# Performance work log

Measured on AMD Instinct MI355X. Metric: run time of the kernel, lower is better.

The kernel has to match this reference:

```python
import jax, jax.numpy as jnp
import numpy as np

B, S, D_MODEL = 8, 1024, 1024
N_HEADS, N_KV_HEADS, HEAD_DIM = 16, 8, 64
ROPE_THETA = 10000.0
LN_EPS = 1e-12


def setup_inputs() -> dict:
    key = jax.random.key(0)
    ks = jax.random.split(key, 6)
    sc = 0.02
    return {
        "hidden_states": jax.random.normal(ks[0], (B, S, D_MODEL), jnp.float32),
        "Wq": jax.random.normal(ks[1], (D_MODEL, N_HEADS * HEAD_DIM), jnp.float32) * sc,
        "bq": jnp.zeros((N_HEADS * HEAD_DIM,), jnp.float32),
        "Wk": jax.random.normal(ks[2], (D_MODEL, N_KV_HEADS * HEAD_DIM), jnp.float32) * sc,
        "bk": jnp.zeros((N_KV_HEADS * HEAD_DIM,), jnp.float32),
        "Wv": jax.random.normal(ks[3], (D_MODEL, N_KV_HEADS * HEAD_DIM), jnp.float32) * sc,
        "bv": jnp.zeros((N_KV_HEADS * HEAD_DIM,), jnp.float32),
        "Wo": jax.random.normal(ks[4], (N_HEADS * HEAD_DIM, D_MODEL), jnp.float32) * sc,
        "bo": jnp.zeros((D_MODEL,), jnp.float32),
        "ln_gamma": jnp.ones((D_MODEL,), jnp.float32),
        "ln_beta": jnp.zeros((D_MODEL,), jnp.float32),
    }


def _rope_tables(seq_len, dim, dtype):
    # lucidrains RotaryEmbedding: inv_freq over even indices, interleaved pairs
    inv_freq = 1.0 / (ROPE_THETA ** (jnp.arange(0, dim, 2, dtype=jnp.float32) / dim))
    angles = jnp.arange(seq_len, dtype=jnp.float32)[:, None] * inv_freq[None, :]  # [S, dim/2]
    return jnp.cos(angles).astype(dtype), jnp.sin(angles).astype(dtype)


def _apply_rope(x, cos, sin):
    # x: [B, S, H, D]; rotate interleaved pairs (x0,x1),(x2,x3),...
    x1 = x[..., 0::2]
    x2 = x[..., 1::2]
    c = cos[None, :, None, :]
    s = sin[None, :, None, :]
    y1 = x1 * c - x2 * s
    y2 = x1 * s + x2 * c
    return jnp.stack([y1, y2], axis=-1).reshape(x.shape)


def reference(hidden_states, Wq, bq, Wk, bk, Wv, bv, Wo, bo, ln_gamma, ln_beta):
    b, s, _ = hidden_states.shape
    q = (hidden_states @ Wq + bq).reshape(b, s, N_HEADS, HEAD_DIM)
    k = (hidden_states @ Wk + bk).reshape(b, s, N_KV_HEADS, HEAD_DIM)
    v = (hidden_states @ Wv + bv).reshape(b, s, N_KV_HEADS, HEAD_DIM)

    cos, sin = _rope_tables(s, HEAD_DIM, hidden_states.dtype)
    q = _apply_rope(q, cos, sin)
    k = _apply_rope(k, cos, sin)

    # GQA: repeat_interleave kv heads to match query heads (factor 2)
    rep = N_HEADS // N_KV_HEADS
    k = jnp.repeat(k, rep, axis=2)  # [B, S, H, D]
    v = jnp.repeat(v, rep, axis=2)

    scale = 1.0 / jnp.sqrt(jnp.asarray(HEAD_DIM, hidden_states.dtype))
    scores = jnp.einsum('bqhd,bkhd->bhqk', q * scale, k)  # [B, H, S, S]
    probs = jax.nn.softmax(scores, axis=-1)
    attn = jnp.einsum('bhqk,bkhd->bqhd', probs, v).reshape(b, s, N_HEADS * HEAD_DIM)

    out = attn @ Wo + bo
    resid = out + hidden_states
    mu = jnp.mean(resid, axis=-1, keepdims=True)
    var = jnp.mean(jnp.square(resid - mu), axis=-1, keepdims=True)
    normed = (resid - mu) * jax.lax.rsqrt(var + LN_EPS)
    return normed * ln_gamma + ln_beta
```

## Files before the change

kernel.cpp:

```cpp
#include <hip/hip_runtime.h>
#include <math.h>
#include <stdint.h>

typedef unsigned short u16;
typedef __bf16 bf16x8 __attribute__((ext_vector_type(8)));
typedef float f32x4 __attribute__((ext_vector_type(4)));

typedef const __attribute__((address_space(1))) void gv_t;
typedef __attribute__((address_space(3))) void lv_t;

__device__ __forceinline__ u16 f2bf(float f) {
    unsigned u = __builtin_bit_cast(unsigned, f);
    return (u16)((u + 0x7FFFu + ((u >> 16) & 1u)) >> 16);
}
__device__ __forceinline__ float bf2f(u16 h) {
    return __builtin_bit_cast(float, (unsigned)h << 16);
}
__device__ __forceinline__ void gll16(const void* g, void* l) {
    __builtin_amdgcn_global_load_lds((gv_t*)(uintptr_t)g,
                                     (lv_t*)(unsigned)(uintptr_t)l, 16, 0, 0);
}

__global__ __launch_bounds__(256) void cvt_bf16_kernel(
    const float* __restrict__ in, u16* __restrict__ out, int n4)
{
    int i = blockIdx.x * 256 + threadIdx.x;
    if (i >= n4) return;
    float4 f = ((const float4*)in)[i];
    ushort4 o = make_ushort4(f2bf(f.x), f2bf(f.y), f2bf(f.z), f2bf(f.w));
    ((ushort4*)out)[i] = o;
}

__global__ __launch_bounds__(256) void cvt_t4_kernel(
    const float* __restrict__ w0, const float* __restrict__ w1,
    const float* __restrict__ w2, const float* __restrict__ w3,
    u16* __restrict__ o0, u16* __restrict__ o1,
    u16* __restrict__ o2, u16* __restrict__ o3)
{
    __shared__ u16 t[64][65];
    const float* in; u16* out; int N;
    switch (blockIdx.z) {
        case 0: in = w0; out = o0; N = 1024; break;
        case 1: in = w1; out = o1; N = 512;  break;
        case 2: in = w2; out = o2; N = 512;  break;
        default: in = w3; out = o3; N = 1024; break;
    }
    int kb = blockIdx.y * 64, nb = blockIdx.x * 64;
    if (nb >= N) return;
    int tid = threadIdx.x;
#pragma unroll
    for (int c = 0; c < 16; ++c) {
        int id = c * 256 + tid;
        int r = id >> 6, n = id & 63;
        t[n][r] = f2bf(in[(size_t)(kb + r) * N + nb + n]);
    }
    __syncthreads();
#pragma unroll
    for (int c = 0; c < 16; ++c) {
        int id = c * 256 + tid;
        int r = id >> 6, n = id & 63;
        out[(size_t)(nb + r) * 1024 + kb + n] = t[r][n];
    }
}

template<int MODE>
__global__ __launch_bounds__(256) void gemm_mfma(
    const u16* __restrict__ A, const u16* __restrict__ Bt,
    const float* __restrict__ b0, const float* __restrict__ b1,
    const float* __restrict__ b2,
    const float* __restrict__ resid, float* __restrict__ Cf,
    u16* __restrict__ Qo, u16* __restrict__ Ko, u16* __restrict__ Vto,
    int N, int K)
{
    __shared__ __align__(16) u16 Asl[128 * 64];
    __shared__ __align__(16) u16 Bsl[128 * 64];
    const int tid = threadIdx.x, lane = tid & 63, w = tid >> 6;
    const int quad = lane >> 4, l16 = lane & 15;
    const int bm = blockIdx.y * 128, bn = blockIdx.x * 128;
    const int wm = (w >> 1) * 64, wn = (w & 1) * 64;

    f32x4 acc[4][4] = {};

    const int dr = lane >> 3;
    const int dcs = (((lane & 7) ^ dr) << 3);
    const u16* Ag = &A[(size_t)(bm + w * 32 + dr) * K + dcs];
    const u16* Bg = &Bt[(size_t)(bn + w * 32 + dr) * K + dcs];
    u16* Al = &Asl[(w * 32) * 64];
    u16* Bl = &Bsl[(w * 32) * 64];

    const int sw = l16 & 7;

    for (int k0 = 0; k0 < K; k0 += 64) {
#pragma unroll
        for (int c = 0; c < 4; ++c) {
            gll16(Ag + (size_t)(c * 8) * K + k0, Al + c * 8 * 64);
            gll16(Bg + (size_t)(c * 8) * K + k0, Bl + c * 8 * 64);
        }
        __syncthreads();
        bf16x8 af[4][2], bfr[4][2];
#pragma unroll
        for (int i = 0; i < 4; ++i)
#pragma unroll
            for (int ks = 0; ks < 2; ++ks)
                af[i][ks] = *(const bf16x8*)&Asl[(wm + i * 16 + l16) * 64 + (((ks * 4 + quad) ^ sw) << 3)];
#pragma unroll
        for (int j = 0; j < 4; ++j)
#pragma unroll
            for (int ks = 0; ks < 2; ++ks)
                bfr[j][ks] = *(const bf16x8*)&Bsl[(wn + j * 16 + l16) * 64 + (((ks * 4 + quad) ^ sw) << 3)];
#pragma unroll
        for (int i = 0; i < 4; ++i)
#pragma unroll
            for (int j = 0; j < 4; ++j)
#pragma unroll
                for (int ks = 0; ks < 2; ++ks)
                    acc[i][j] = __builtin_amdgcn_mfma_f32_16x16x32_bf16(af[i][ks], bfr[j][ks], acc[i][j], 0, 0, 0);
        __syncthreads();
    }

#pragma unroll
    for (int j = 0; j < 4; ++j) {
        int col = bn + wn + j * 16 + l16;
        if (MODE == 1) {
            float bb = b0[col];
#pragma unroll
            for (int i = 0; i < 4; ++i) {
                int row0 = bm + wm + i * 16 + quad * 4;
#pragma unroll
                for (int r = 0; r < 4; ++r) {
                    size_t off = (size_t)(row0 + r) * N + col;
                    Cf[off] = acc[i][j][r] + bb + resid[off];
                }
            }
        } else if (col < 1024) {
            float bb = b0[col];
#pragma unroll
            for (int i = 0; i < 4; ++i) {
                int row0 = bm + wm + i * 16 + quad * 4;
#pragma unroll
                for (int r = 0; r < 4; ++r)
                    Qo[(size_t)(row0 + r) * 1024 + col] = f2bf(acc[i][j][r] + bb);
            }
        } else if (col < 1536) {
            int c2 = col - 1024;
            float bb = b1[c2];
#pragma unroll
            for (int i = 0; i < 4; ++i) {
                int row0 = bm + wm + i * 16 + quad * 4;
#pragma unroll
                for (int r = 0; r < 4; ++r)
                    Ko[(size_t)(row0 + r) * 512 + c2] = f2bf(acc[i][j][r] + bb);
            }
        } else {
            int c2 = col - 1536, kvh = c2 >> 6, d = c2 & 63;
            float bb = b2[c2];
#pragma unroll
            for (int i = 0; i < 4; ++i) {
                int row0 = bm + wm + i * 16 + quad * 4;
                int b = row0 >> 10, s = row0 & 1023;
                ushort4 o4;
                o4.x = f2bf(acc[i][j][0] + bb);
                o4.y = f2bf(acc[i][j][1] + bb);
                o4.z = f2bf(acc[i][j][2] + bb);
                o4.w = f2bf(acc[i][j][3] + bb);
                *(ushort4*)&Vto[(size_t)((b * 8 + kvh) * 64 + d) * 1024 + s] = o4;
            }
        }
    }
}

__global__ __launch_bounds__(256) void rope_bf16_kernel(
    u16* __restrict__ x, int shift, int stride, int total)
{
    int idx = blockIdx.x * 256 + threadIdx.x;
    if (idx >= total) return;
    int j = idx & 31;
    int h = (idx >> 5) & ((1 << shift) - 1);
    int row = idx >> (5 + shift);
    int pos = row & 1023;
    float inv = exp2f((float)j * -0.4152410118609203f);
    float sn, cs;
    sincosf((float)pos * inv, &sn, &cs);
    unsigned* p = (unsigned*)&x[(size_t)row * stride + h * 64 + (j << 1)];
    unsigned u = *p;
    float x1 = bf2f((u16)(u & 0xffff)), x2 = bf2f((u16)(u >> 16));
    float y1 = x1 * cs - x2 * sn, y2 = x1 * sn + x2 * cs;
    *p = (unsigned)f2bf(y1) | ((unsigned)f2bf(y2) << 16);
}

__global__ __launch_bounds__(256, 4) void attn_mfma(
    const u16* __restrict__ Q, const u16* __restrict__ K,
    const u16* __restrict__ Vt, u16* __restrict__ O)
{
    __shared__ __align__(16) u16 Ks[2][64 * 64];
    __shared__ __align__(16) u16 Vts[2][64 * 64];
    __shared__ __align__(16) u16 Ps[64][40];

    const int tid = threadIdx.x, lane = tid & 63, w = tid >> 6;
    const int quad = lane >> 4, l16 = lane & 15;
    const int id = blockIdx.x;
    const int nid = (id & 7) * 128 + (id >> 3);
    const int qt = nid & 7, h = (nid >> 3) & 15, b = nid >> 7;
    const int kvh = h >> 1;
    const size_t qrow0 = (size_t)b * 1024 + qt * 128;
    const size_t krow0 = (size_t)b * 1024;
    const u16* Vg = Vt + (size_t)((b * 8 + kvh) * 64) * 1024;

    const int dr = lane >> 3;
    const int dcs = (((lane & 7) ^ dr) << 3);
    const u16* Kg0 = &K[(krow0 + w * 16 + dr) * 512 + kvh * 64 + dcs];
    const u16* Vg0 = &Vg[(size_t)(w * 16 + dr) * 1024 + dcs];
    const int sw = l16 & 7;
    const float C1 = 0.18033688011112043f;

#pragma unroll
    for (int c = 0; c < 2; ++c) {
        gll16(Kg0 + (size_t)(c * 8) * 512, &Ks[0][(w * 16 + c * 8) * 64]);
        gll16(Vg0 + (size_t)(c * 8) * 1024, &Vts[0][(w * 16 + c * 8) * 64]);
    }

    bf16x8 qf[2][2];
#pragma unroll
    for (int qg = 0; qg < 2; ++qg) {
        int qrow = w * 32 + qg * 16 + l16;
        float fpos = (float)(qt * 128 + qrow);
#pragma unroll
        for (int ks = 0; ks < 2; ++ks) {
            uint4 qraw = *(const uint4*)&Q[(qrow0 + qrow) * 1024 + h * 64 + ks * 32 + quad * 8];
            unsigned o_[4];
#pragma unroll
            for (int t = 0; t < 4; ++t) {
                int j = ks * 16 + quad * 4 + t;
                float inv = exp2f((float)j * -0.4152410118609203f);
                float sn_, cs_;
                sincosf(fpos * inv, &sn_, &cs_);
                cs_ *= C1; sn_ *= C1;
                unsigned u = (&qraw.x)[t];
                float x1 = bf2f((u16)(u & 0xffff)), x2 = bf2f((u16)(u >> 16));
                float y1 = x1 * cs_ - x2 * sn_, y2 = x1 * sn_ + x2 * cs_;
                o_[t] = (unsigned)f2bf(y1) | ((unsigned)f2bf(y2) << 16);
            }
            qf[qg][ks] = __builtin_bit_cast(bf16x8, make_uint4(o_[0], o_[1], o_[2], o_[3]));
        }
    }

    f32x4 acc_o[2][4] = {};
    f32x4 lsum[2] = {};
    const bf16x8 ones = __builtin_bit_cast(bf16x8,
        make_uint4(0x3F803F80u, 0x3F803F80u, 0x3F803F80u, 0x3F803F80u));

    for (int kt = 0; kt < 16; ++kt) {
        const int cur = kt & 1;
        __syncthreads();

        if (kt < 15) {
#pragma unroll
            for (int c = 0; c < 2; ++c) {
                gll16(Kg0 + (size_t)((kt + 1) * 64 + c * 8) * 512,
                      &Ks[cur ^ 1][(w * 16 + c * 8) * 64]);
                gll16(Vg0 + (size_t)(c * 8) * 1024 + (kt + 1) * 64,
                      &Vts[cur ^ 1][(w * 16 + c * 8) * 64]);
            }
        }

        f32x4 s[2][4] = {};
        __builtin_amdgcn_s_setprio(1);
#pragma unroll
        for (int ks = 0; ks < 2; ++ks) {
#pragma unroll
            for (int nt = 0; nt < 4; ++nt) {
                bf16x8 ak = *(const bf16x8*)&Ks[cur][(nt * 16 + l16) * 64 + (((ks * 4 + quad) ^ sw) << 3)];
                s[0][nt] = __builtin_amdgcn_mfma_f32_16x16x32_bf16(ak, qf[0][ks], s[0][nt], 0, 0, 0);
                s[1][nt] = __builtin_amdgcn_mfma_f32_16x16x32_bf16(ak, qf[1][ks], s[1][nt], 0, 0, 0);
            }
        }
        __builtin_amdgcn_s_setprio(0);

#pragma unroll
        for (int kc = 0; kc < 2; ++kc) {
            bf16x8 av[4];
#pragma unroll
            for (int nt = 0; nt < 4; ++nt)
                av[nt] = *(const bf16x8*)&Vts[cur][(nt * 16 + l16) * 64 + (((kc * 4 + quad) ^ sw) << 3)];
#pragma unroll
            for (int qg = 0; qg < 2; ++qg) {
#pragma unroll
                for (int ntl = 0; ntl < 2; ++ntl) {
                    int nt = kc * 2 + ntl;
                    float p0 = __builtin_amdgcn_exp2f(s[qg][nt][0]);
                    float p1 = __builtin_amdgcn_exp2f(s[qg][nt][1]);
                    unsigned pk0 = __builtin_amdgcn_perm(
                        __builtin_bit_cast(unsigned, p1),
                        __builtin_bit_cast(unsigned, p0), 0x07060302u);
                    float p2 = __builtin_amdgcn_exp2f(s[qg][nt][2]);
                    float p3 = __builtin_amdgcn_exp2f(s[qg][nt][3]);
                    unsigned pk1 = __builtin_amdgcn_perm(
                        __builtin_bit_cast(unsigned, p3),
                        __builtin_bit_cast(unsigned, p2), 0x07060302u);
                    *(uint2*)&Ps[w * 16 + l16][ntl * 16 + quad * 4] = make_uint2(pk0, pk1);
                }
                bf16x8 bp = *(const bf16x8*)&Ps[w * 16 + l16][quad * 8];
                __builtin_amdgcn_s_setprio(1);
                lsum[qg] = __builtin_amdgcn_mfma_f32_16x16x32_bf16(ones, bp, lsum[qg], 0, 0, 0);
#pragma unroll
                for (int nt = 0; nt < 4; ++nt)
                    acc_o[qg][nt] = __builtin_amdgcn_mfma_f32_16x16x32_bf16(av[nt], bp, acc_o[qg][nt], 0, 0, 0);
                __builtin_amdgcn_s_setprio(0);
            }
        }
    }

#pragma unroll
    for (int qg = 0; qg < 2; ++qg) {
        float rl = 1.0f / lsum[qg][0];
        size_t orow = (qrow0 + w * 32 + qg * 16 + l16) * 1024 + h * 64;
#pragma unroll
        for (int nt = 0; nt < 4; ++nt) {
            ushort4 o4;
            o4.x = f2bf(acc_o[qg][nt][0] * rl);
            o4.y = f2bf(acc_o[qg][nt][1] * rl);
            o4.z = f2bf(acc_o[qg][nt][2] * rl);
            o4.w = f2bf(acc_o[qg][nt][3] * rl);
            *(ushort4*)&O[orow + nt * 16 + quad * 4] = o4;
        }
    }
}

__global__ __launch_bounds__(256) void ln_kernel(float* __restrict__ io,
    const float* __restrict__ gamma, const float* __restrict__ beta)
{
    int row = blockIdx.x;
    int tid = threadIdx.x;
    float* p = io + (size_t)row * 1024;
    float4 x = *reinterpret_cast<const float4*>(&p[tid << 2]);
    float s = x.x + x.y + x.z + x.w;
    float ss = fmaf(x.x, x.x, fmaf(x.y, x.y, fmaf(x.z, x.z, x.w * x.w)));
#pragma unroll
    for (int off = 32; off > 0; off >>= 1) {
        s  += __shfl_down(s, off);
        ss += __shfl_down(ss, off);
    }
    __shared__ float rs[4], rss[4];
    int lane = tid & 63, wid = tid >> 6;
    if (lane == 0) { rs[wid] = s; rss[wid] = ss; }
    __syncthreads();
    float S = rs[0] + rs[1] + rs[2] + rs[3];
    float SS = rss[0] + rss[1] + rss[2] + rss[3];
    float mu = S * (1.0f / 1024.0f);
    float var = SS * (1.0f / 1024.0f) - mu * mu;
    float rstd = rsqrtf(var + 1e-12f);
    float4 g = *reinterpret_cast<const float4*>(&gamma[tid << 2]);
    float4 be = *reinterpret_cast<const float4*>(&beta[tid << 2]);
    float4 o;
    o.x = (x.x - mu) * rstd * g.x + be.x;
    o.y = (x.y - mu) * rstd * g.y + be.y;
    o.z = (x.z - mu) * rstd * g.z + be.z;
    o.w = (x.w - mu) * rstd * g.w + be.w;
    *reinterpret_cast<float4*>(&p[tid << 2]) = o;
}

extern "C" void kernel_launch(void* const* d_in, const int* in_sizes, int n_in,
                              void* d_out, int out_size, void* d_ws, size_t ws_size,
                              hipStream_t stream)
{
    (void)in_sizes; (void)n_in; (void)out_size; (void)ws_size;
    const float* hidden = (const float*)d_in[0];
    const float* Wq = (const float*)d_in[1];
    const float* bq = (const float*)d_in[2];
    const float* Wk = (const float*)d_in[3];
    const float* bk = (const float*)d_in[4];
    const float* Wv = (const float*)d_in[5];
    const float* bv = (const float*)d_in[6];
    const float* Wo = (const float*)d_in[7];
    const float* bo = (const float*)d_in[8];
    const float* g  = (const float*)d_in[9];
    const float* be = (const float*)d_in[10];
    float* out = (float*)d_out;

    u16* hb  = (u16*)d_ws;
    u16* Wqt = hb  + (size_t)8192 * 1024;
    u16* Wkt = Wqt + (size_t)1024 * 1024;
    u16* Wvt = Wkt + (size_t)512 * 1024;
    u16* Wot = Wvt + (size_t)512 * 1024;
    u16* Qb  = Wot + (size_t)1024 * 1024;
    u16* Kb  = Qb  + (size_t)8192 * 1024;
    u16* Vtb = Kb  + (size_t)8192 * 512;

    cvt_bf16_kernel<<<8192, 256, 0, stream>>>(hidden, hb, 8192 * 1024 / 4);
    cvt_t4_kernel<<<dim3(16, 16, 4), 256, 0, stream>>>(Wq, Wk, Wv, Wo, Wqt, Wkt, Wvt, Wot);

    gemm_mfma<0><<<dim3(16, 64), 256, 0, stream>>>(hb, Wqt, bq, bk, bv,
        nullptr, nullptr, Qb, Kb, Vtb, 2048, 1024);

    rope_bf16_kernel<<<8192, 256, 0, stream>>>(Kb, 3, 512, 8192 * 8 * 32);

    attn_mfma<<<dim3(1024), 256, 0, stream>>>(Qb, Kb, Vtb, Qb);

    gemm_mfma<1><<<dim3(8, 64), 256, 0, stream>>>(Qb, Wot, bo, nullptr, nullptr,
        hidden, out, nullptr, nullptr, nullptr, 1024, 1024);
    ln_kernel<<<8192, 256, 0, stream>>>(out, g, be);
}
```

Before: 249.9 us.

## Double-buffer GEMM LDS tiles and remap block IDs for XCD locality

The QKV and output GEMMs now use two LDS buffers, so the async global-to-LDS load of the next K tile is issued while MFMAs run on the current one, with one barrier per iteration instead of two. A 1D grid with an XCD-aware block ID remap, chunking consecutive tiles per id&7 group, is meant to improve L2 reuse across the chiplets. LDS per block doubles to 64KB, which may lower occupancy.

```diff
diff --git a/kernel.cpp b/kernel.cpp
--- a/kernel.cpp
+++ b/kernel.cpp
@@ -63,8 +63,8 @@
     }
 }
 
-template<int MODE>
-__global__ __launch_bounds__(256) void gemm_mfma(
+template<int MODE, int NBX>
+__device__ __forceinline__ void gemm_body(
     const u16* __restrict__ A, const u16* __restrict__ Bt,
     const float* __restrict__ b0, const float* __restrict__ b1,
     const float* __restrict__ b2,
@@ -72,11 +72,15 @@
     u16* __restrict__ Qo, u16* __restrict__ Ko, u16* __restrict__ Vto,
     int N, int K)
 {
-    __shared__ __align__(16) u16 Asl[128 * 64];
-    __shared__ __align__(16) u16 Bsl[128 * 64];
+    __shared__ __align__(16) u16 Asl[2][128 * 64];
+    __shared__ __align__(16) u16 Bsl[2][128 * 64];
     const int tid = threadIdx.x, lane = tid & 63, w = tid >> 6;
     const int quad = lane >> 4, l16 = lane & 15;
-    const int bm = blockIdx.y * 128, bn = blockIdx.x * 128;
+    const int id = blockIdx.x;
+    const int chunk = (NBX * 64) >> 3;
+    const int nid = (id & 7) * chunk + (id >> 3);
+    const int bx = nid & (NBX - 1), by = nid / NBX;
+    const int bm = by * 128, bn = bx * 128;
     const int wm = (w >> 1) * 64, wn = (w & 1) * 64;
 
     f32x4 acc[4][4] = {};
@@ -85,29 +89,37 @@
     const int dcs = (((lane & 7) ^ dr) << 3);
     const u16* Ag = &A[(size_t)(bm + w * 32 + dr) * K + dcs];
     const u16* Bg = &Bt[(size_t)(bn + w * 32 + dr) * K + dcs];
-    u16* Al = &Asl[(w * 32) * 64];
-    u16* Bl = &Bsl[(w * 32) * 64];
 
     const int sw = l16 & 7;
 
-    for (int k0 = 0; k0 < K; k0 += 64) {
-#pragma unroll
-        for (int c = 0; c < 4; ++c) {
-            gll16(Ag + (size_t)(c * 8) * K + k0, Al + c * 8 * 64);
-            gll16(Bg + (size_t)(c * 8) * K + k0, Bl + c * 8 * 64);
-        }
+    const int NT = K >> 6;
+#pragma unroll
+    for (int c = 0; c < 4; ++c) {
+        gll16(Ag + (size_t)(c * 8) * K, &Asl[0][(w * 32 + c * 8) * 64]);
+        gll16(Bg + (size_t)(c * 8) * K, &Bsl[0][(w * 32 + c * 8) * 64]);
+    }
+    for (int t = 0; t < NT; ++t) {
+        const int cur = t & 1;
         __syncthreads();
+        if (t < NT - 1) {
+            const int k0 = (t + 1) * 64;
+#pragma unroll
+            for (int c = 0; c < 4; ++c) {
+                gll16(Ag + (size_t)(c * 8) * K + k0, &Asl[cur ^ 1][(w * 32 + c * 8) * 64]);
+                gll16(Bg + (size_t)(c * 8) * K + k0, &Bsl[cur ^ 1][(w * 32 + c * 8) * 64]);
+            }
+        }
         bf16x8 af[4][2], bfr[4][2];
 #pragma unroll
         for (int i = 0; i < 4; ++i)
 #pragma unroll
             for (int ks = 0; ks < 2; ++ks)
-                af[i][ks] = *(const bf16x8*)&Asl[(wm + i * 16 + l16) * 64 + (((ks * 4 + quad) ^ sw) << 3)];
+                af[i][ks] = *(const bf16x8*)&Asl[cur][(wm + i * 16 + l16) * 64 + (((ks * 4 + quad) ^ sw) << 3)];
 #pragma unroll
         for (int j = 0; j < 4; ++j)
 #pragma unroll
             for (int ks = 0; ks < 2; ++ks)
-                bfr[j][ks] = *(const bf16x8*)&Bsl[(wn + j * 16 + l16) * 64 + (((ks * 4 + quad) ^ sw) << 3)];
+                bfr[j][ks] = *(const bf16x8*)&Bsl[cur][(wn + j * 16 + l16) * 64 + (((ks * 4 + quad) ^ sw) << 3)];
 #pragma unroll
         for (int i = 0; i < 4; ++i)
 #pragma unroll
@@ -115,7 +127,6 @@
 #pragma unroll
                 for (int ks = 0; ks < 2; ++ks)
                     acc[i][j] = __builtin_amdgcn_mfma_f32_16x16x32_bf16(af[i][ks], bfr[j][ks], acc[i][j], 0, 0, 0);
-        __syncthreads();
     }
 
 #pragma unroll
@@ -167,6 +178,24 @@
             }
         }
     }
+}
+
+__global__ __launch_bounds__(256) void gemm_qkv(
+    const u16* __restrict__ A, const u16* __restrict__ Bt,
+    const float* __restrict__ b0, const float* __restrict__ b1,
+    const float* __restrict__ b2,
+    u16* __restrict__ Qo, u16* __restrict__ Ko, u16* __restrict__ Vto)
+{
+    gemm_body<0, 16>(A, Bt, b0, b1, b2, nullptr, nullptr, Qo, Ko, Vto, 2048, 1024);
+}
+
+__global__ __launch_bounds__(256) void gemm_out(
+    const u16* __restrict__ A, const u16* __restrict__ Bt,
+    const float* __restrict__ b0,
+    const float* __restrict__ resid, float* __restrict__ Cf)
+{
+    gemm_body<1, 8>(A, Bt, b0, nullptr, nullptr, resid, Cf,
+                    nullptr, nullptr, nullptr, 1024, 1024);
 }
 
 __global__ __launch_bounds__(256) void rope_bf16_kernel(
@@ -389,14 +418,13 @@
     cvt_bf16_kernel<<<8192, 256, 0, stream>>>(hidden, hb, 8192 * 1024 / 4);
     cvt_t4_kernel<<<dim3(16, 16, 4), 256, 0, stream>>>(Wq, Wk, Wv, Wo, Wqt, Wkt, Wvt, Wot);
 
-    gemm_mfma<0><<<dim3(16, 64), 256, 0, stream>>>(hb, Wqt, bq, bk, bv,
-        nullptr, nullptr, Qb, Kb, Vtb, 2048, 1024);
+    gemm_qkv<<<dim3(1024), 256, 0, stream>>>(hb, Wqt, bq, bk, bv, Qb, Kb, Vtb);
 
     rope_bf16_kernel<<<8192, 256, 0, stream>>>(Kb, 3, 512, 8192 * 8 * 32);
 
     attn_mfma<<<dim3(1024), 256, 0, stream>>>(Qb, Kb, Vtb, Qb);
 
-    gemm_mfma<1><<<dim3(8, 64), 256, 0, stream>>>(Qb, Wot, bo, nullptr, nullptr,
-        hidden, out, nullptr, nullptr, nullptr, 1024, 1024);
+    gemm_out<<<dim3(512), 256, 0, stream>>>(Qb, Wot, bo, hidden, out);
+
     ln_kernel<<<8192, 256, 0, stream>>>(out, g, be);
 }
```

After: 235.4 us. 1.06x faster.
